# Kernel tuning notes

Measured on AMD Instinct MI355X. Metric: run time of the kernel, lower is better.

## Reference

```python
import jax, jax.numpy as jnp
import numpy as np

DECAY = 0.99
EPS = 1e-05


def setup_inputs() -> dict:
    key = jax.random.key(0)
    k1, k2 = jax.random.split(key)
    B, L, D, K = 8, 2048, 512, 4096
    x = jax.random.normal(k1, (B, L, D), dtype=jnp.float32)
    # variance_scaling(scale=1, fan_in, uniform): U(-limit, limit), limit = sqrt(3/fan_in)
    limit = np.sqrt(3.0 / D)
    codebook = jax.random.uniform(k2, (K, D), dtype=jnp.float32, minval=-limit, maxval=limit)
    return {
        "x": x,
        "codebook": codebook,
        "hidden_cluster": jnp.zeros((K,), jnp.float32),
        "hidden_dw": jnp.zeros((K, D), jnp.float32),
        "count": jnp.zeros((), jnp.float32),
    }


def reference(x, codebook, hidden_cluster, hidden_dw, count):
    K, D = codebook.shape
    B, L, _ = x.shape
    # avoids materializing the (B,L,K,D) broadcast the naive cdist creates)
    x2 = jnp.sum(x * x, axis=-1, keepdims=True)                  # (B,L,1)
    c2 = jnp.sum(codebook * codebook, axis=-1)                   # (K,)
    xc = jnp.einsum("bld,kd->blk", x, codebook)                  # (B,L,K)
    d2 = x2 - 2.0 * xc + c2
    indices = jnp.argmin(d2, axis=-1)                            # (B,L) int
    flat_idx = indices.reshape(-1)

    # cluster_counts = one_hot(indices).sum((0,1)) as a scatter-add
    cluster_counts = jnp.zeros((K,), jnp.float32).at[flat_idx].add(1.0)
    # dw = einsum('bln,bld->nd', one_hot, x) as a scatter-add of x rows
    dw = jnp.zeros((K, D), jnp.float32).at[flat_idx].add(x.reshape(-1, D))

    decay = jnp.asarray(DECAY, x.dtype)
    one = jnp.ones([], x.dtype)
    count_new = count + 1.0
    bias = one - decay ** count_new

    hidden_cluster_new = hidden_cluster * decay + (one - decay) * cluster_counts
    avg_cluster = hidden_cluster_new / bias
    hidden_dw_new = hidden_dw * decay + (one - decay) * dw
    avg_dw = hidden_dw_new / bias

    N = jnp.sum(avg_cluster)
    cc = (avg_cluster + EPS) / (N + K * EPS) * N
    codebook_new = avg_dw / cc[:, None]

    # quantized = one_hot(indices) @ codebook_new == gather
    q = codebook_new[indices]                                    # (B,L,D)
    quantized = x + jax.lax.stop_gradient(q - x)
    # optax.l2_loss(x, quantized).mean() == 0.5*(x-quantized)^2 mean
    codebook_loss = 0.5 * jnp.mean(jnp.square(x - quantized))
    return quantized, codebook_loss, indices
```

## Files before the change

kernel.cpp:

```cpp
#include <hip/hip_runtime.h>
#include <math.h>

#define BL 16384
#define D  512
#define K  4096
#define NCHB 8
#define XLOFF 8388608

#define OFF_C2    0
#define OFF_X2    (16<<10)
#define OFF_CNT   (80<<10)
#define OFF_AVGC  (96<<10)
#define OFF_SCAL  (112<<10)
#define OFF_IDX16 (116<<10)
#define OFF_KEYS  (160<<10)
#define OFF_CAND  (288<<10)
#define OFF_CBP   (576<<10)
#define OFF_CBN_FB (256<<10)

typedef _Float16 f16x8 __attribute__((ext_vector_type(8)));
typedef float    f32x4 __attribute__((ext_vector_type(4)));
#define MFMA16(a,b,c) __builtin_amdgcn_mfma_f32_16x16x32_f16(a,b,c,0,0,0)


__global__ void rowsq_all(const float* __restrict__ x, const float* __restrict__ cb,
                          float* __restrict__ x2, float* __restrict__ c2)
{
    int b    = blockIdx.x;
    int lane = threadIdx.x;
    const float* p; float* o; int row;
    if (b < K) { p = cb; o = c2; row = b; }
    else       { p = x;  o = x2; row = b - K; }
    p += (size_t)row * D;
    float s = 0.f;
#pragma unroll
    for (int j = 0; j < D / 64; ++j) {
        float v = p[lane + j * 64];
        s = fmaf(v, v, s);
    }
#pragma unroll
    for (int off = 32; off > 0; off >>= 1)
        s += __shfl_down(s, off, 64);
    if (lane == 0) o[row] = s;
}

__global__ __launch_bounds__(256) void rescore_kernel(
    const float* __restrict__ x, const float* __restrict__ cb,
    const float* __restrict__ x2, const float* __restrict__ c2,
    const unsigned short* __restrict__ cand,
    unsigned long long* __restrict__ keys,
    float* __restrict__ counts, unsigned short* __restrict__ idx16)
{
    int t = blockIdx.x * 256 + threadIdx.x;
    int row = t >> 3, ci = t & 7;
    int idx = cand[(size_t)row * 8 + ci];
    const float* xp = x  + (size_t)row * D;
    const float* cp = cb + (size_t)idx * D;
    float acc = 0.f;
#pragma unroll 4
    for (int k0 = 0; k0 < D; k0 += 4) {
        float4 xv = *(const float4*)(xp + k0);
        float4 cv = *(const float4*)(cp + k0);
        acc = fmaf(xv.x, cv.x, acc);
        acc = fmaf(xv.y, cv.y, acc);
        acc = fmaf(xv.z, cv.z, acc);
        acc = fmaf(xv.w, cv.w, acc);
    }
    float wv = x2[row] - 2.0f * acc;
    float dd = wv + c2[idx];
    unsigned long long key =
        ((unsigned long long)__float_as_uint(dd) << 12) | (unsigned long long)idx;
#pragma unroll
    for (int m = 1; m < 8; m <<= 1) {
        unsigned long long o = __shfl_xor(key, m, 64);
        key = o < key ? o : key;
    }
    if ((t & 7) == 0) {
        keys[row] = key;
        int kf = (int)(key & 0xFFFULL);
        idx16[row] = (unsigned short)kf;
        atomicAdd(&counts[kf], 1.0f);
    }
}


__device__ __forceinline__ void load_lds16(const unsigned short* g, unsigned short* l) {
    __builtin_amdgcn_global_load_lds(
        (const __attribute__((address_space(1))) unsigned int*)(g),
        (__attribute__((address_space(3))) unsigned int*)(l), 16, 0, 0);
}

__global__ __launch_bounds__(256) void split_interleave(
    const float* __restrict__ x, const float* __restrict__ cb,
    unsigned short* __restrict__ xp, unsigned short* __restrict__ cbp)
{
    int gw   = blockIdx.x * 4 + (threadIdx.x >> 6);
    int lane = threadIdx.x & 63;
    int rl   = lane >> 3;
    int p    = lane & 7;
    const float* src; int nr, c, r0; bool isX;
    if (gw < 16384) { c = gw >> 11; r0 = (gw & 2047) * 8; src = x;  nr = BL; isX = true; }
    else { int lw = gw - 16384; c = lw >> 9; r0 = (lw & 511) * 8; src = cb; nr = K; isX = false; }
    int r = r0 + rl;
    int g = p ^ rl;
    const float* sp = src + (size_t)r * D + c * 64 + g * 8;
    float4 f0 = *(const float4*)sp, f1 = *(const float4*)(sp + 4);
    float f[8] = {f0.x,f0.y,f0.z,f0.w,f1.x,f1.y,f1.z,f1.w};
    __align__(16) _Float16 oh[8], ol[8];
#pragma unroll
    for (int i = 0; i < 8; ++i) {
        _Float16 h = (_Float16)f[i];
        oh[i] = h;
        ol[i] = (_Float16)(f[i] - (float)h);
    }
    size_t off = ((size_t)(c * nr + r) * 8 + p) * 8;
    if (isX) {
        *(uint4*)(xp + off)         = *(const uint4*)oh;
        *(uint4*)(xp + XLOFF + off) = *(const uint4*)ol;
    } else {
        *(uint4*)(cbp + off) = *(const uint4*)oh;
    }
}

__global__ __launch_bounds__(256, 2) void argmin_mfma(
    const unsigned short* __restrict__ xp, const unsigned short* __restrict__ cbp,
    const float* __restrict__ x2, const float* __restrict__ c2,
    unsigned short* __restrict__ cand)
{
    __shared__ __align__(16) unsigned short sAh[128 * 64];
    __shared__ __align__(16) unsigned short sAl[128 * 64];
    __shared__ __align__(16) unsigned short sB [128 * 64];

    const int tid = threadIdx.x;
    const int l   = tid & 63;
    const int w   = tid >> 6;
    const int wm  = w >> 1, wn = w & 1;
    const int q   = l >> 4;
    const int cc  = l & 15;
    const int row0 = blockIdx.x * 128;
    const int nb   = blockIdx.y * 1024;

    int rdA[4], rdB[4];
#pragma unroll
    for (int t = 0; t < 4; ++t) {
        int ra = wm * 64 + t * 16 + cc;
        int rb = wn * 64 + t * 16 + cc;
        rdA[t] = ra * 128 + ((q ^ (ra & 7)) * 16);
        rdB[t] = rb * 128 + ((q ^ (rb & 7)) * 16);
    }

    unsigned long long k1[16], k2[16];
#pragma unroll
    for (int s = 0; s < 16; ++s) { k1[s] = ~0ULL; k2[s] = ~0ULL; }

    for (int n0 = 0; n0 < 8; ++n0) {
        f32x4 acc[4][4];
#pragma unroll
        for (int tm = 0; tm < 4; ++tm)
#pragma unroll
            for (int tn = 0; tn < 4; ++tn) { f32x4 z = {0.f,0.f,0.f,0.f}; acc[tm][tn] = z; }

        for (int c = 0; c < NCHB; ++c) {
            __syncthreads();
            {
                size_t abase = ((size_t)c * BL + row0) * 64;
                size_t bbase = ((size_t)c * K + nb + n0 * 128) * 64;
#pragma unroll
                for (int i = 0; i < 12; ++i) {
                    int gi = i * 4 + w;
                    if (gi < 16)
                        load_lds16(xp + abase + gi * 512 + l * 8, &sAh[gi * 512 + l * 8]);
                    else if (gi < 32) {
                        int ga = gi - 16;
                        load_lds16(xp + XLOFF + abase + ga * 512 + l * 8, &sAl[ga * 512 + l * 8]);
                    } else {
                        int gb = gi - 32;
                        load_lds16(cbp + bbase + gb * 512 + l * 8, &sB[gb * 512 + l * 8]);
                    }
                }
            }
            __syncthreads();
#pragma unroll
            for (int kh = 0; kh < 2; ++kh) {
                const int xo = kh * 64;
                f16x8 Ah[4], Al[4], Bf[4];
#pragma unroll
                for (int t = 0; t < 4; ++t) {
                    Ah[t] = *(const f16x8*)((const char*)sAh + (rdA[t] ^ xo));
                    Al[t] = *(const f16x8*)((const char*)sAl + (rdA[t] ^ xo));
                    Bf[t] = *(const f16x8*)((const char*)sB  + (rdB[t] ^ xo));
                }
#pragma unroll
                for (int tm = 0; tm < 4; ++tm)
#pragma unroll
                    for (int tn = 0; tn < 4; ++tn) {
                        acc[tm][tn] = MFMA16(Ah[tm], Bf[tn], acc[tm][tn]);
                        acc[tm][tn] = MFMA16(Al[tm], Bf[tn], acc[tm][tn]);
                    }
            }
        }
        float c2v[4];
#pragma unroll
        for (int tn = 0; tn < 4; ++tn)
            c2v[tn] = c2[nb + n0 * 128 + wn * 64 + tn * 16 + cc];
#pragma unroll
        for (int tm = 0; tm < 4; ++tm)
#pragma unroll
            for (int r = 0; r < 4; ++r) {
                int s = tm * 4 + r;
                float x2v = x2[row0 + wm * 64 + tm * 16 + q * 4 + r];
#pragma unroll
                for (int tn = 0; tn < 4; ++tn) {
                    unsigned col = nb + n0 * 128 + wn * 64 + tn * 16 + cc;
                    float dd = (x2v - 2.0f * acc[tm][tn][r]) + c2v[tn];
                    unsigned long long key =
                        ((unsigned long long)__float_as_uint(dd) << 12) | col;
                    if (key < k1[s]) { k2[s] = k1[s]; k1[s] = key; }
                    else if (key < k2[s]) { k2[s] = key; }
                }
            }
    }

#pragma unroll
    for (int s = 0; s < 16; ++s) {
#pragma unroll
        for (int m = 1; m < 16; m <<= 1) {
            unsigned long long o1 = __shfl_xor(k1[s], m, 64);
            unsigned long long o2 = __shfl_xor(k2[s], m, 64);
            unsigned long long lf = k1[s] > o1 ? k1[s] : o1;
            unsigned long long ws_ = k2[s] < o2 ? k2[s] : o2;
            k1[s] = k1[s] < o1 ? k1[s] : o1;
            k2[s] = lf < ws_ ? lf : ws_;
        }
    }

    __syncthreads();
    unsigned long long* sc = (unsigned long long*)sAh;
    if (cc == 0) {
#pragma unroll
        for (int s = 0; s < 16; ++s) {
            int rl = wm * 64 + (s >> 2) * 16 + q * 4 + (s & 3);
            sc[(rl * 2 + wn) * 2 + 0] = k1[s];
            sc[(rl * 2 + wn) * 2 + 1] = k2[s];
        }
    }
    __syncthreads();
    if (tid < 128) {
        unsigned long long pa1 = sc[(tid * 2 + 0) * 2 + 0], pa2 = sc[(tid * 2 + 0) * 2 + 1];
        unsigned long long pb1 = sc[(tid * 2 + 1) * 2 + 0], pb2 = sc[(tid * 2 + 1) * 2 + 1];
        unsigned long long m1 = pa1 < pb1 ? pa1 : pb1;
        unsigned long long lf = pa1 > pb1 ? pa1 : pb1;
        unsigned long long ws_ = pa2 < pb2 ? pa2 : pb2;
        unsigned long long m2 = lf < ws_ ? lf : ws_;
        size_t base = (size_t)(row0 + tid) * 8 + blockIdx.y * 2;
        cand[base + 0] = (unsigned short)(m1 & 0xFFFULL);
        cand[base + 1] = (unsigned short)(m2 & 0xFFFULL);
    }
}

__global__ __launch_bounds__(256) void argmin_fb(
    const float* __restrict__ x, const float* __restrict__ cb,
    const float* __restrict__ x2, const float* __restrict__ c2,
    unsigned long long* __restrict__ keys)
{
    __shared__ __align__(16) float As[32][68];
    __shared__ __align__(16) float Bs[32][68];
    __shared__ float rv[64][16];
    __shared__ int   ri[64][16];

    const int tid  = threadIdx.x;
    const int tx   = tid & 15;
    const int ty   = tid >> 4;
    const int row0 = blockIdx.x * 64;
    const int nb   = blockIdx.y * 1024;

    float x2r[4];
#pragma unroll
    for (int m = 0; m < 4; ++m) x2r[m] = x2[row0 + ty * 4 + m];

    float minv[4]; int mini[4];
#pragma unroll
    for (int m = 0; m < 4; ++m) { minv[m] = 3.4028235e38f; mini[m] = 0; }

    for (int n0 = 0; n0 < 1024; n0 += 64) {
        float acc[4][4];
#pragma unroll
        for (int m = 0; m < 4; ++m)
#pragma unroll
            for (int n = 0; n < 4; ++n) acc[m][n] = 0.f;

        for (int d0 = 0; d0 < D; d0 += 32) {
            __syncthreads();
#pragma unroll
            for (int j = 0; j < 2; ++j) {
                int v   = j * 256 + tid;
                int row = v >> 3;
                int col = (v & 7) * 4;
                float4 av = *(const float4*)(x  + (size_t)(row0 + row) * D + d0 + col);
                As[col + 0][row] = av.x; As[col + 1][row] = av.y;
                As[col + 2][row] = av.z; As[col + 3][row] = av.w;
                float4 bv = *(const float4*)(cb + (size_t)(nb + n0 + row) * D + d0 + col);
                Bs[col + 0][row] = bv.x; Bs[col + 1][row] = bv.y;
                Bs[col + 2][row] = bv.z; Bs[col + 3][row] = bv.w;
            }
            __syncthreads();
#pragma unroll
            for (int kk = 0; kk < 32; ++kk) {
                float4 a4 = *(const float4*)&As[kk][ty * 4];
                float4 b4 = *(const float4*)&Bs[kk][tx * 4];
                float a_[4] = { a4.x, a4.y, a4.z, a4.w };
                float b_[4] = { b4.x, b4.y, b4.z, b4.w };
#pragma unroll
                for (int m = 0; m < 4; ++m)
#pragma unroll
                    for (int n = 0; n < 4; ++n)
                        acc[m][n] = fmaf(a_[m], b_[n], acc[m][n]);
            }
        }
#pragma unroll
        for (int n = 0; n < 4; ++n) {
            int kidx = nb + n0 + tx * 4 + n;
            float c2k = c2[kidx];
#pragma unroll
            for (int m = 0; m < 4; ++m) {
                float wv = x2r[m] - 2.0f * acc[m][n];
                float dd = wv + c2k;
                if (dd < minv[m]) { minv[m] = dd; mini[m] = kidx; }
            }
        }
    }
#pragma unroll
    for (int m = 0; m < 4; ++m) { rv[ty * 4 + m][tx] = minv[m]; ri[ty * 4 + m][tx] = mini[m]; }
    __syncthreads();
    if (tid < 64) {
        float bv = rv[tid][0]; int bi = ri[tid][0];
#pragma unroll
        for (int j = 1; j < 16; ++j) {
            float v = rv[tid][j]; int ii = ri[tid][j];
            if (v < bv || (v == bv && ii < bi)) { bv = v; bi = ii; }
        }
        unsigned long long key =
            ((unsigned long long)__float_as_uint(bv) << 12) | (unsigned long long)bi;
        atomicMin(&keys[row0 + tid], key);
    }
}


__global__ void count_kernel(const unsigned long long* __restrict__ keys,
                             float* __restrict__ counts, unsigned short* __restrict__ idx16)
{
    int i = blockIdx.x * 256 + threadIdx.x;
    int k = (int)(keys[i] & 0xFFFULL);
    idx16[i] = (unsigned short)k;
    atomicAdd(&counts[k], 1.0f);
}

__global__ __launch_bounds__(256) void ema_cluster_kernel(
    const float* __restrict__ hc, const float* __restrict__ counts,
    const float* __restrict__ countp, float* __restrict__ avgc, float* __restrict__ Nout)
{
    __shared__ float sm[256];
    int i = blockIdx.x * 256 + threadIdx.x;
    const float om = 1.0f - 0.99f;
    float bias = 1.0f - powf(0.99f, countp[0] + 1.0f);
    float a = (hc[i] * 0.99f + om * counts[i]) / bias;
    avgc[i] = a;
    sm[threadIdx.x] = a;
    __syncthreads();
    for (int s = 128; s > 0; s >>= 1) {
        if (threadIdx.x < s) sm[threadIdx.x] += sm[threadIdx.x + s];
        __syncthreads();
    }
    if (threadIdx.x == 0) atomicAdd(Nout, sm[0]);
}

__global__ __launch_bounds__(256) void code_update_kernel(
    const float* __restrict__ x, const unsigned short* __restrict__ idx16,
    const float* __restrict__ hdw, const float* __restrict__ avgc,
    const float* __restrict__ Nptr, const float* __restrict__ countp,
    float* __restrict__ cbn)
{
    __shared__ unsigned short rows[2048];
    __shared__ int cnt;
    int k = blockIdx.x, tid = threadIdx.x;
    if (tid == 0) cnt = 0;
    __syncthreads();
    const uint4* ip = (const uint4*)idx16;
    for (int j = 0; j < 8; ++j) {
        int u = j * 256 + tid;
        uint4 v = ip[u];
        unsigned ww[4] = {v.x, v.y, v.z, v.w};
#pragma unroll
        for (int e = 0; e < 4; ++e) {
            int k0 = (int)(ww[e] & 0xFFFFu), k1 = (int)(ww[e] >> 16);
            if (k0 == k) { int p = atomicAdd(&cnt, 1); if (p < 2048) rows[p] = (unsigned short)(u * 8 + e * 2); }
            if (k1 == k) { int p = atomicAdd(&cnt, 1); if (p < 2048) rows[p] = (unsigned short)(u * 8 + e * 2 + 1); }
        }
    }
    __syncthreads();
    int n = cnt < 2048 ? cnt : 2048;
    float a0 = 0.f, a1 = 0.f;
    for (int p = 0; p < n; ++p) {
        int r = rows[p];
        a0 += x[(size_t)r * D + tid];
        a1 += x[(size_t)r * D + tid + 256];
    }
    const float om = 1.0f - 0.99f;
    float bias = 1.0f - powf(0.99f, countp[0] + 1.0f);
    float Nv = *Nptr;
    float ccv = ((avgc[k] + 1e-5f) / (Nv + 0.04096f)) * Nv;
    size_t b = (size_t)k * D;
    cbn[b + tid]       = ((hdw[b + tid]       * 0.99f + om * a0) / bias) / ccv;
    cbn[b + tid + 256] = ((hdw[b + tid + 256] * 0.99f + om * a1) / bias) / ccv;
}

__global__ __launch_bounds__(256) void gather_kernel(
    const float* __restrict__ x, const unsigned long long* __restrict__ keys,
    const float* __restrict__ cbn, float* __restrict__ outq,
    float* __restrict__ partial)
{
    __shared__ float sm[256];
    int row = blockIdx.x;
    int tid = threadIdx.x;
    int k   = (int)(keys[row] & 0xFFFULL);
    const float* xpp = x   + (size_t)row * D;
    const float* cp  = cbn + (size_t)k   * D;
    float* op = outq + (size_t)row * D;
    float local = 0.f;
#pragma unroll
    for (int j = 0; j < 2; ++j) {
        int d = tid + j * 256;
        float xv = xpp[d];
        float qv = cp[d];
        float quant = xv + (qv - xv);
        op[d] = quant;
        float diff = xv - quant;
        local = fmaf(diff, diff, local);
    }
    sm[tid] = local;
    __syncthreads();
    for (int s = 128; s > 0; s >>= 1) {
        if (tid < s) sm[tid] += sm[tid + s];
        __syncthreads();
    }
    if (tid == 0) {
        partial[row] = sm[0];
        outq[8388609 + row] = (float)k;
    }
}

__global__ __launch_bounds__(256) void finalize_kernel(
    const float* __restrict__ partial, float* __restrict__ out)
{
    __shared__ double sm[256];
    int tid = threadIdx.x;
    double s = 0.0;
#pragma unroll
    for (int j = 0; j < 64; ++j) s += (double)partial[tid + j * 256];
    sm[tid] = s;
    __syncthreads();
    for (int st = 128; st > 0; st >>= 1) {
        if (tid < st) sm[tid] += sm[tid + st];
        __syncthreads();
    }
    if (tid == 0) out[8388608] = (float)(0.5 * sm[0] / 8388608.0);
}


extern "C" void kernel_launch(void* const* d_in, const int* in_sizes, int n_in,
                              void* d_out, int out_size, void* d_ws, size_t ws_size,
                              hipStream_t stream)
{
    const float* x   = (const float*)d_in[0];
    const float* cb  = (const float*)d_in[1];
    const float* hc  = (const float*)d_in[2];
    const float* hdw = (const float*)d_in[3];
    const float* cnt = (const float*)d_in[4];
    float* out = (float*)d_out;

    char* ws = (char*)d_ws;
    float*  c2     = (float*)(ws + OFF_C2);
    float*  x2     = (float*)(ws + OFF_X2);
    float*  counts = (float*)(ws + OFF_CNT);
    float*  avgc   = (float*)(ws + OFF_AVGC);
    float*  Nout   = (float*)(ws + OFF_SCAL + 8);
    unsigned short* idx16 = (unsigned short*)(ws + OFF_IDX16);
    unsigned long long* keys = (unsigned long long*)(ws + OFF_KEYS);
    float*  partial= (float*)(ws + OFF_X2);

    hipMemsetAsync(ws + OFF_CNT, 0, (32 << 10) + 16, stream);

    rowsq_all<<<K + BL, 64, 0, stream>>>(x, cb, x2, c2);

    const bool primary = ws_size >= ((size_t)10 << 20);
    float* cbn;
    if (primary) {
        unsigned short* gxp = (unsigned short*)d_out;
        unsigned short* gcp = (unsigned short*)(ws + OFF_CBP);
        unsigned short* cand = (unsigned short*)(ws + OFF_CAND);
        cbn = (float*)(ws + OFF_CBP);

        split_interleave<<<5120, 256, 0, stream>>>(x, cb, gxp, gcp);
        argmin_mfma<<<dim3(BL / 128, 4), 256, 0, stream>>>(gxp, gcp, x2, c2, cand);
        rescore_kernel<<<(BL * 8) / 256, 256, 0, stream>>>(x, cb, x2, c2, cand, keys,
                                                           counts, idx16);
    } else {
        cbn = (float*)(ws + OFF_CBN_FB);
        hipMemsetAsync(ws + OFF_KEYS, 0xFF, BL * 8, stream);
        argmin_fb<<<dim3(BL / 64, 4), 256, 0, stream>>>(x, cb, x2, c2, keys);
        count_kernel<<<BL / 256, 256, 0, stream>>>(keys, counts, idx16);
    }

    ema_cluster_kernel<<<K / 256, 256, 0, stream>>>(hc, counts, cnt, avgc, Nout);
    code_update_kernel<<<K, 256, 0, stream>>>(x, idx16, hdw, avgc, Nout, cnt, cbn);
    gather_kernel<<<BL, 256, 0, stream>>>(x, keys, cbn, out, partial);
    finalize_kernel<<<1, 256, 0, stream>>>(partial, out);
}
```

Before: 334.2 us.

## Fuse rowsq into split, widen argmin grid, batch code update and gather

Merges the row-norm kernel into the fp16 split/interleave kernel so one launch covers both. The MFMA argmin grid now uses 8 column blocks of 512 codes, which doubles the candidates per row to 16, and the rescore kernel checks all 16. The code update kernel handles 4 codes per block so the idx16 scan is shared, and the gather kernel uses one wave per row with float4 accesses and a shuffle reduction. More parallelism in argmin comes at the cost of twice the rescore work, and the larger candidate buffer moves the packed codebook offset.

```diff
diff --git a/kernel.cpp b/kernel.cpp
--- a/kernel.cpp
+++ b/kernel.cpp
@@ -15,7 +15,7 @@
 #define OFF_IDX16 (116<<10)
 #define OFF_KEYS  (160<<10)
 #define OFF_CAND  (288<<10)
-#define OFF_CBP   (576<<10)
+#define OFF_CBP   (832<<10)
 #define OFF_CBN_FB (256<<10)
 
 typedef _Float16 f16x8 __attribute__((ext_vector_type(8)));
@@ -52,8 +52,8 @@
     float* __restrict__ counts, unsigned short* __restrict__ idx16)
 {
     int t = blockIdx.x * 256 + threadIdx.x;
-    int row = t >> 3, ci = t & 7;
-    int idx = cand[(size_t)row * 8 + ci];
+    int row = t >> 4, ci = t & 15;
+    int idx = cand[(size_t)row * 16 + ci];
     const float* xp = x  + (size_t)row * D;
     const float* cp = cb + (size_t)idx * D;
     float acc = 0.f;
@@ -71,11 +71,11 @@
     unsigned long long key =
         ((unsigned long long)__float_as_uint(dd) << 12) | (unsigned long long)idx;
 #pragma unroll
-    for (int m = 1; m < 8; m <<= 1) {
+    for (int m = 1; m < 16; m <<= 1) {
         unsigned long long o = __shfl_xor(key, m, 64);
         key = o < key ? o : key;
     }
-    if ((t & 7) == 0) {
+    if ((t & 15) == 0) {
         keys[row] = key;
         int kf = (int)(key & 0xFFFULL);
         idx16[row] = (unsigned short)kf;
@@ -90,35 +90,57 @@
         (__attribute__((address_space(3))) unsigned int*)(l), 16, 0, 0);
 }
 
-__global__ __launch_bounds__(256) void split_interleave(
+__global__ __launch_bounds__(256) void rowsq_split(
     const float* __restrict__ x, const float* __restrict__ cb,
-    unsigned short* __restrict__ xp, unsigned short* __restrict__ cbp)
-{
-    int gw   = blockIdx.x * 4 + (threadIdx.x >> 6);
-    int lane = threadIdx.x & 63;
-    int rl   = lane >> 3;
-    int p    = lane & 7;
-    const float* src; int nr, c, r0; bool isX;
-    if (gw < 16384) { c = gw >> 11; r0 = (gw & 2047) * 8; src = x;  nr = BL; isX = true; }
-    else { int lw = gw - 16384; c = lw >> 9; r0 = (lw & 511) * 8; src = cb; nr = K; isX = false; }
-    int r = r0 + rl;
-    int g = p ^ rl;
-    const float* sp = src + (size_t)r * D + c * 64 + g * 8;
-    float4 f0 = *(const float4*)sp, f1 = *(const float4*)(sp + 4);
-    float f[8] = {f0.x,f0.y,f0.z,f0.w,f1.x,f1.y,f1.z,f1.w};
-    __align__(16) _Float16 oh[8], ol[8];
-#pragma unroll
-    for (int i = 0; i < 8; ++i) {
-        _Float16 h = (_Float16)f[i];
-        oh[i] = h;
-        ol[i] = (_Float16)(f[i] - (float)h);
-    }
-    size_t off = ((size_t)(c * nr + r) * 8 + p) * 8;
-    if (isX) {
-        *(uint4*)(xp + off)         = *(const uint4*)oh;
-        *(uint4*)(xp + XLOFF + off) = *(const uint4*)ol;
+    unsigned short* __restrict__ xp, unsigned short* __restrict__ cbp,
+    float* __restrict__ x2, float* __restrict__ c2)
+{
+    int blk = blockIdx.x;
+    if (blk < 5120) {
+        int gw   = blk * 4 + (threadIdx.x >> 6);
+        int lane = threadIdx.x & 63;
+        int rl   = lane >> 3;
+        int p    = lane & 7;
+        const float* src; int nr, c, r0; bool isX;
+        if (gw < 16384) { c = gw >> 11; r0 = (gw & 2047) * 8; src = x;  nr = BL; isX = true; }
+        else { int lw = gw - 16384; c = lw >> 9; r0 = (lw & 511) * 8; src = cb; nr = K; isX = false; }
+        int r = r0 + rl;
+        int g = p ^ rl;
+        const float* sp = src + (size_t)r * D + c * 64 + g * 8;
+        float4 f0 = *(const float4*)sp, f1 = *(const float4*)(sp + 4);
+        float f[8] = {f0.x,f0.y,f0.z,f0.w,f1.x,f1.y,f1.z,f1.w};
+        __align__(16) _Float16 oh[8], ol[8];
+#pragma unroll
+        for (int i = 0; i < 8; ++i) {
+            _Float16 h = (_Float16)f[i];
+            oh[i] = h;
+            ol[i] = (_Float16)(f[i] - (float)h);
+        }
+        size_t off = ((size_t)(c * nr + r) * 8 + p) * 8;
+        if (isX) {
+            *(uint4*)(xp + off)         = *(const uint4*)oh;
+            *(uint4*)(xp + XLOFF + off) = *(const uint4*)ol;
+        } else {
+            *(uint4*)(cbp + off) = *(const uint4*)oh;
+        }
     } else {
-        *(uint4*)(cbp + off) = *(const uint4*)oh;
+        int w    = threadIdx.x >> 6;
+        int lane = threadIdx.x & 63;
+        int b    = (blk - 5120) * 4 + w;
+        const float* p; float* o; int row;
+        if (b < K) { p = cb; o = c2; row = b; }
+        else       { p = x;  o = x2; row = b - K; }
+        p += (size_t)row * D;
+        float s = 0.f;
+#pragma unroll
+        for (int j = 0; j < D / 64; ++j) {
+            float v = p[lane + j * 64];
+            s = fmaf(v, v, s);
+        }
+#pragma unroll
+        for (int off = 32; off > 0; off >>= 1)
+            s += __shfl_down(s, off, 64);
+        if (lane == 0) o[row] = s;
     }
 }
 
@@ -138,7 +160,7 @@
     const int q   = l >> 4;
     const int cc  = l & 15;
     const int row0 = blockIdx.x * 128;
-    const int nb   = blockIdx.y * 1024;
+    const int nb   = blockIdx.y * 512;
 
     int rdA[4], rdB[4];
 #pragma unroll
@@ -153,7 +175,7 @@
 #pragma unroll
     for (int s = 0; s < 16; ++s) { k1[s] = ~0ULL; k2[s] = ~0ULL; }
 
-    for (int n0 = 0; n0 < 8; ++n0) {
+    for (int n0 = 0; n0 < 4; ++n0) {
         f32x4 acc[4][4];
 #pragma unroll
         for (int tm = 0; tm < 4; ++tm)
@@ -252,7 +274,7 @@
         unsigned long long lf = pa1 > pb1 ? pa1 : pb1;
         unsigned long long ws_ = pa2 < pb2 ? pa2 : pb2;
         unsigned long long m2 = lf < ws_ ? lf : ws_;
-        size_t base = (size_t)(row0 + tid) * 8 + blockIdx.y * 2;
+        size_t base = (size_t)(row0 + tid) * 16 + blockIdx.y * 2;
         cand[base + 0] = (unsigned short)(m1 & 0xFFFULL);
         cand[base + 1] = (unsigned short)(m2 & 0xFFFULL);
     }
@@ -380,10 +402,10 @@
     const float* __restrict__ Nptr, const float* __restrict__ countp,
     float* __restrict__ cbn)
 {
-    __shared__ unsigned short rows[2048];
-    __shared__ int cnt;
-    int k = blockIdx.x, tid = threadIdx.x;
-    if (tid == 0) cnt = 0;
+    __shared__ unsigned short rows[4][2048];
+    __shared__ int cnt[4];
+    int k0 = blockIdx.x * 4, tid = threadIdx.x;
+    if (tid < 4) cnt[tid] = 0;
     __syncthreads();
     const uint4* ip = (const uint4*)idx16;
     for (int j = 0; j < 8; ++j) {
@@ -392,26 +414,31 @@
         unsigned ww[4] = {v.x, v.y, v.z, v.w};
 #pragma unroll
         for (int e = 0; e < 4; ++e) {
-            int k0 = (int)(ww[e] & 0xFFFFu), k1 = (int)(ww[e] >> 16);
-            if (k0 == k) { int p = atomicAdd(&cnt, 1); if (p < 2048) rows[p] = (unsigned short)(u * 8 + e * 2); }
-            if (k1 == k) { int p = atomicAdd(&cnt, 1); if (p < 2048) rows[p] = (unsigned short)(u * 8 + e * 2 + 1); }
-        }
-    }
-    __syncthreads();
-    int n = cnt < 2048 ? cnt : 2048;
-    float a0 = 0.f, a1 = 0.f;
-    for (int p = 0; p < n; ++p) {
-        int r = rows[p];
-        a0 += x[(size_t)r * D + tid];
-        a1 += x[(size_t)r * D + tid + 256];
-    }
+            unsigned d0 = (ww[e] & 0xFFFFu) - (unsigned)k0;
+            unsigned d1 = (ww[e] >> 16)     - (unsigned)k0;
+            if (d0 < 4u) { int p = atomicAdd(&cnt[d0], 1); if (p < 2048) rows[d0][p] = (unsigned short)(u * 8 + e * 2); }
+            if (d1 < 4u) { int p = atomicAdd(&cnt[d1], 1); if (p < 2048) rows[d1][p] = (unsigned short)(u * 8 + e * 2 + 1); }
+        }
+    }
+    __syncthreads();
     const float om = 1.0f - 0.99f;
     float bias = 1.0f - powf(0.99f, countp[0] + 1.0f);
     float Nv = *Nptr;
-    float ccv = ((avgc[k] + 1e-5f) / (Nv + 0.04096f)) * Nv;
-    size_t b = (size_t)k * D;
-    cbn[b + tid]       = ((hdw[b + tid]       * 0.99f + om * a0) / bias) / ccv;
-    cbn[b + tid + 256] = ((hdw[b + tid + 256] * 0.99f + om * a1) / bias) / ccv;
+#pragma unroll
+    for (int c = 0; c < 4; ++c) {
+        int k = k0 + c;
+        int n = cnt[c] < 2048 ? cnt[c] : 2048;
+        float a0 = 0.f, a1 = 0.f;
+        for (int p = 0; p < n; ++p) {
+            int r = rows[c][p];
+            a0 += x[(size_t)r * D + tid];
+            a1 += x[(size_t)r * D + tid + 256];
+        }
+        float ccv = ((avgc[k] + 1e-5f) / (Nv + 0.04096f)) * Nv;
+        size_t b = (size_t)k * D;
+        cbn[b + tid]       = ((hdw[b + tid]       * 0.99f + om * a0) / bias) / ccv;
+        cbn[b + tid + 256] = ((hdw[b + tid + 256] * 0.99f + om * a1) / bias) / ccv;
+    }
 }
 
 __global__ __launch_bounds__(256) void gather_kernel(
@@ -419,32 +446,32 @@
     const float* __restrict__ cbn, float* __restrict__ outq,
     float* __restrict__ partial)
 {
-    __shared__ float sm[256];
-    int row = blockIdx.x;
-    int tid = threadIdx.x;
-    int k   = (int)(keys[row] & 0xFFFULL);
+    int w    = threadIdx.x >> 6;
+    int lane = threadIdx.x & 63;
+    int row  = blockIdx.x * 4 + w;
+    int k    = (int)(keys[row] & 0xFFFULL);
     const float* xpp = x   + (size_t)row * D;
     const float* cp  = cbn + (size_t)k   * D;
     float* op = outq + (size_t)row * D;
     float local = 0.f;
 #pragma unroll
     for (int j = 0; j < 2; ++j) {
-        int d = tid + j * 256;
-        float xv = xpp[d];
-        float qv = cp[d];
-        float quant = xv + (qv - xv);
-        op[d] = quant;
-        float diff = xv - quant;
-        local = fmaf(diff, diff, local);
-    }
-    sm[tid] = local;
-    __syncthreads();
-    for (int s = 128; s > 0; s >>= 1) {
-        if (tid < s) sm[tid] += sm[tid + s];
-        __syncthreads();
-    }
-    if (tid == 0) {
-        partial[row] = sm[0];
+        int d = j * 256 + lane * 4;
+        float4 xv = *(const float4*)(xpp + d);
+        float4 qv = *(const float4*)(cp + d);
+        float4 qq;
+        qq.x = xv.x + (qv.x - xv.x); qq.y = xv.y + (qv.y - xv.y);
+        qq.z = xv.z + (qv.z - xv.z); qq.w = xv.w + (qv.w - xv.w);
+        *(float4*)(op + d) = qq;
+        float dx = xv.x - qq.x, dy = xv.y - qq.y, dz = xv.z - qq.z, dw = xv.w - qq.w;
+        local = fmaf(dx, dx, local); local = fmaf(dy, dy, local);
+        local = fmaf(dz, dz, local); local = fmaf(dw, dw, local);
+    }
+#pragma unroll
+    for (int off = 32; off > 0; off >>= 1)
+        local += __shfl_down(local, off, 64);
+    if (lane == 0) {
+        partial[row] = local;
         outq[8388609 + row] = (float)k;
     }
 }
@@ -490,8 +517,6 @@
 
     hipMemsetAsync(ws + OFF_CNT, 0, (32 << 10) + 16, stream);
 
-    rowsq_all<<<K + BL, 64, 0, stream>>>(x, cb, x2, c2);
-
     const bool primary = ws_size >= ((size_t)10 << 20);
     float* cbn;
     if (primary) {
@@ -500,19 +525,20 @@
         unsigned short* cand = (unsigned short*)(ws + OFF_CAND);
         cbn = (float*)(ws + OFF_CBP);
 
-        split_interleave<<<5120, 256, 0, stream>>>(x, cb, gxp, gcp);
-        argmin_mfma<<<dim3(BL / 128, 4), 256, 0, stream>>>(gxp, gcp, x2, c2, cand);
-        rescore_kernel<<<(BL * 8) / 256, 256, 0, stream>>>(x, cb, x2, c2, cand, keys,
-                                                           counts, idx16);
+        rowsq_split<<<10240, 256, 0, stream>>>(x, cb, gxp, gcp, x2, c2);
+        argmin_mfma<<<dim3(BL / 128, 8), 256, 0, stream>>>(gxp, gcp, x2, c2, cand);
+        rescore_kernel<<<(BL * 16) / 256, 256, 0, stream>>>(x, cb, x2, c2, cand, keys,
+                                                            counts, idx16);
     } else {
         cbn = (float*)(ws + OFF_CBN_FB);
         hipMemsetAsync(ws + OFF_KEYS, 0xFF, BL * 8, stream);
+        rowsq_all<<<K + BL, 64, 0, stream>>>(x, cb, x2, c2);
         argmin_fb<<<dim3(BL / 64, 4), 256, 0, stream>>>(x, cb, x2, c2, keys);
         count_kernel<<<BL / 256, 256, 0, stream>>>(keys, counts, idx16);
     }
 
     ema_cluster_kernel<<<K / 256, 256, 0, stream>>>(hc, counts, cnt, avgc, Nout);
-    code_update_kernel<<<K, 256, 0, stream>>>(x, idx16, hdw, avgc, Nout, cnt, cbn);
-    gather_kernel<<<BL, 256, 0, stream>>>(x, keys, cbn, out, partial);
+    code_update_kernel<<<K / 4, 256, 0, stream>>>(x, idx16, hdw, avgc, Nout, cnt, cbn);
+    gather_kernel<<<BL / 4, 256, 0, stream>>>(x, keys, cbn, out, partial);
     finalize_kernel<<<1, 256, 0, stream>>>(partial, out);
 }
```

Result: slower. 367.7 us (+10.1%).
